# Kernel tuning notes

Measured on AMD Instinct MI355X. Metric: run time of the kernel, lower is better.

## Reference

```python
import jax, jax.numpy as jnp
import numpy as np

MAX_DISP = 48
PATCH = 3
OFFSET = 0
PAD = PATCH // 2
EPS = 1e-3


def _unfold(x, P, pad):
    # x: [B,C,H,W] -> [B,C,K2,H,W], K2 enumerated row-major over the PxP window
    B, C, H, W = x.shape
    xp = jnp.pad(x, ((0, 0), (0, 0), (pad, pad), (pad, pad)))
    return jnp.stack([xp[:, :, i:i + H, j:j + W]
                      for i in range(P) for j in range(P)], axis=2)


def _normalize(x, axes):
    # torch F.normalize: x / clamp(||x||_2, min=eps)
    n = jnp.sqrt(jnp.sum(x * x, axis=axes, keepdims=True))
    return x / jnp.maximum(n, EPS)


def setup_inputs() -> dict:
    key = jax.random.key(0)
    k1, k2, k3 = jax.random.split(key, 3)
    shp = (2, 32, 128, 416)
    return {
        "xl": jax.random.normal(k1, shp, dtype=jnp.float32),
        "xm": jax.random.normal(k2, shp, dtype=jnp.float32),
        "xr": jax.random.normal(k3, shp, dtype=jnp.float32),
    }


def reference(xl, xm, xr):
    B, C, H, W = xl.shape
    K2 = PATCH * PATCH
    scale = (C * K2) ** 0.5

    pl = _normalize(_unfold(xl, PATCH, PAD), (1, 2))  # [B,C,K2,H,W]
    pr = _normalize(_unfold(xr, PATCH, PAD), (1, 2))
    fl = _normalize(xm, (1,))                          # [B,C,H,W]

    # fl is constant over the K2 axis, so sum patches over K2 once for sim_L/sim_R
    Sl = pl.sum(axis=2)  # [B,C,H,W]
    Sr = pr.sum(axis=2)

    cL, cR, cLR = [], [], []
    for d in range(OFFSET, OFFSET + MAX_DISP):
        if d > 0:
            # shifted_l[w] = patches_l[w+d] (zero right pad); shifted_r[w] = patches_r[w-d]
            sL = jnp.einsum('bchw,bchw->bhw', fl[..., :W - d], Sl[..., d:])
            sL = jnp.pad(sL, ((0, 0), (0, 0), (0, d)))
            sR = jnp.einsum('bchw,bchw->bhw', fl[..., d:], Sr[..., :W - d])
            sR = jnp.pad(sR, ((0, 0), (0, 0), (d, 0)))
            wlr = W - 2 * d  # overlap region of the two opposite shifts
            if wlr > 0:
                sLR = jnp.einsum('bckhw,bckhw->bhw', pl[..., 2 * d:], pr[..., :wlr])
                sLR = jnp.pad(sLR, ((0, 0), (0, 0), (d, d)))
            else:
                sLR = jnp.zeros((B, H, W), xl.dtype)
        else:
            sL = jnp.einsum('bchw,bchw->bhw', fl, Sl)
            sR = jnp.einsum('bchw,bchw->bhw', fl, Sr)
            sLR = jnp.einsum('bckhw,bckhw->bhw', pl, pr)
        cL.append(sL / scale)
        cR.append(sR / scale)
        cLR.append(sLR / scale)

    cost = jnp.stack([jnp.stack(cL, 1), jnp.stack(cR, 1), jnp.stack(cLR, 1)], axis=1)
    return jnp.clip(cost, -10.0, 10.0).astype(jnp.float16)  # [B,3,D,H,W]
```

## Files before the change

### kernel.cpp

```cpp
#include <hip/hip_runtime.h>
#include <math.h>

#define B 2
#define C 32
#define H 128
#define W 416
#define D 48
#define HW (H*W)
#define CHW (C*HW)
#define EPSN 1e-3f
#define ISCALE 0.05892556509887896f
#define LSTRH 40
#define NDSP 4
#define DSPL (D / NDSP)

typedef _Float16 half2v __attribute__((ext_vector_type(2)));
typedef _Float16 half4v __attribute__((ext_vector_type(4)));
typedef _Float16 half8v __attribute__((ext_vector_type(8)));

#if defined(__has_builtin)
#if __has_builtin(__builtin_amdgcn_fdot2)
#define FDOT2(a, b, c) __builtin_amdgcn_fdot2((a), (b), (c), false)
#endif
#endif
#ifndef FDOT2
#define FDOT2(a, b, c) ((c) + (float)(a)[0] * (float)(b)[0] + (float)(a)[1] * (float)(b)[1])
#endif

__device__ __forceinline__ float clip10(float x) {
    return fminf(fmaxf(x, -10.0f), 10.0f);
}

__global__ __launch_bounds__(256) void k_sq(const float* __restrict__ xl,
                                            const float* __restrict__ xr,
                                            const float* __restrict__ xm,
                                            float* __restrict__ sql,
                                            float* __restrict__ sqr,
                                            float* __restrict__ inm) {
    int idx = blockIdx.x * 256 + threadIdx.x;
    if (idx >= B * HW) return;
    int b = idx / HW, hw = idx - b * HW;
    const float* pl = xl + (size_t)b * CHW + hw;
    const float* pr = xr + (size_t)b * CHW + hw;
    const float* pm = xm + (size_t)b * CHW + hw;
    float al = 0.f, ar = 0.f, am = 0.f;
#pragma unroll
    for (int c = 0; c < C; ++c) {
        float vl = pl[c * HW], vr = pr[c * HW], vm = pm[c * HW];
        al += vl * vl; ar += vr * vr; am += vm * vm;
    }
    sql[idx] = al;
    sqr[idx] = ar;
    inm[idx] = 1.0f / fmaxf(sqrtf(am), EPSN);
}

__global__ __launch_bounds__(256) void k_norm(const float* __restrict__ sql,
                                              const float* __restrict__ sqr,
                                              float* __restrict__ inl,
                                              float* __restrict__ inr) {
    int idx = blockIdx.x * 256 + threadIdx.x;
    if (idx >= B * HW) return;
    int b = idx / HW, hw = idx - b * HW;
    int h = hw / W, w = hw - h * W;
    float sl = 0.f, sr = 0.f;
#pragma unroll
    for (int di = -1; di <= 1; ++di) {
        int hh = h + di;
        if (hh < 0 || hh >= H) continue;
#pragma unroll
        for (int dj = -1; dj <= 1; ++dj) {
            int ww = w + dj;
            if (ww < 0 || ww >= W) continue;
            int p = b * HW + hh * W + ww;
            sl += sql[p];
            sr += sqr[p];
        }
    }
    inl[idx] = 1.0f / fmaxf(sqrtf(sl), EPSN);
    inr[idx] = 1.0f / fmaxf(sqrtf(sr), EPSN);
}

__global__ __launch_bounds__(256) void k_box(const float* __restrict__ xl,
                                             const float* __restrict__ xr,
                                             _Float16* __restrict__ boxl,
                                             _Float16* __restrict__ boxr) {
    int idx = blockIdx.x * 256 + threadIdx.x;
    int w4 = (idx % (W / 4)) * 4;
    int h = (idx / (W / 4)) % H;
    int rest = idx / (H * (W / 4));
    size_t base = (size_t)rest * HW;
    float4 al = {0.f, 0.f, 0.f, 0.f}, ar = {0.f, 0.f, 0.f, 0.f};
#pragma unroll
    for (int dh = -1; dh <= 1; ++dh) {
        int hh = h + dh;
        if (hh < 0 || hh >= H) continue;
        const float* rl = xl + base + hh * W;
        const float* rr = xr + base + hh * W;
        float4 m = *(const float4*)(rl + w4);
        float lm = (w4 > 0) ? rl[w4 - 1] : 0.f;
        float rm = (w4 + 4 < W) ? rl[w4 + 4] : 0.f;
        al.x += lm + m.x + m.y;  al.y += m.x + m.y + m.z;
        al.z += m.y + m.z + m.w; al.w += m.z + m.w + rm;
        float4 n = *(const float4*)(rr + w4);
        float ln = (w4 > 0) ? rr[w4 - 1] : 0.f;
        float rn = (w4 + 4 < W) ? rr[w4 + 4] : 0.f;
        ar.x += ln + n.x + n.y;  ar.y += n.x + n.y + n.z;
        ar.z += n.y + n.z + n.w; ar.w += n.z + n.w + rn;
    }
    half4v ol = {(_Float16)al.x, (_Float16)al.y, (_Float16)al.z, (_Float16)al.w};
    half4v orr = {(_Float16)ar.x, (_Float16)ar.y, (_Float16)ar.z, (_Float16)ar.w};
    *(half4v*)(boxl + base + h * W + w4) = ol;
    *(half4v*)(boxr + base + h * W + w4) = orr;
}

__device__ __forceinline__ void stage_row_h(const _Float16* __restrict__ gsrc,
                                            _Float16* __restrict__ lds,
                                            int tid, int nthreads) {
    for (int t = tid; t < (W / 4) * C; t += nthreads) {
        int rw = t & 7;
        int cl = (t >> 3) & 7;
        int g  = t >> 6;
        int wg = g % 13;
        int ch = g / 13;
        int c  = ch * 8 + cl;
        int w4 = (wg * 8 + rw) * 4;
        half4v v = *(const half4v*)(gsrc + (size_t)c * HW + w4);
        lds[(w4 + 0) * LSTRH + c] = v[0];
        lds[(w4 + 1) * LSTRH + c] = v[1];
        lds[(w4 + 2) * LSTRH + c] = v[2];
        lds[(w4 + 3) * LSTRH + c] = v[3];
    }
}

__device__ __forceinline__ void stage_row_cvt(const float* __restrict__ gsrc,
                                              _Float16* __restrict__ lds,
                                              int tid, int nthreads) {
    for (int t = tid; t < (W / 4) * C; t += nthreads) {
        int rw = t & 7;
        int cl = (t >> 3) & 7;
        int g  = t >> 6;
        int wg = g % 13;
        int ch = g / 13;
        int c  = ch * 8 + cl;
        int w4 = (wg * 8 + rw) * 4;
        float4 v = *(const float4*)(gsrc + (size_t)c * HW + w4);
        lds[(w4 + 0) * LSTRH + c] = (_Float16)v.x;
        lds[(w4 + 1) * LSTRH + c] = (_Float16)v.y;
        lds[(w4 + 2) * LSTRH + c] = (_Float16)v.z;
        lds[(w4 + 3) * LSTRH + c] = (_Float16)v.w;
    }
}

__device__ __forceinline__ float dot16(const half2v* __restrict__ a,
                                       const _Float16* __restrict__ col) {
    const half8v* c8 = (const half8v*)col;
    float s = 0.f;
#pragma unroll
    for (int q = 0; q < 4; ++q) {
        half8v v = c8[q];
#pragma unroll
        for (int i = 0; i < 4; ++i) {
            half2v p = {v[2 * i], v[2 * i + 1]};
            s = FDOT2(a[4 * q + i], p, s);
        }
    }
    return s;
}

__device__ __forceinline__ void dot16x2(const half2v* __restrict__ a0,
                                        const half2v* __restrict__ a1,
                                        const _Float16* __restrict__ col,
                                        float& r0, float& r1) {
    const half8v* c8 = (const half8v*)col;
    float s0 = 0.f, s1 = 0.f;
#pragma unroll
    for (int q = 0; q < 4; ++q) {
        half8v v = c8[q];
#pragma unroll
        for (int i = 0; i < 4; ++i) {
            half2v p = {v[2 * i], v[2 * i + 1]};
            s0 = FDOT2(a0[4 * q + i], p, s0);
            s1 = FDOT2(a1[4 * q + i], p, s1);
        }
    }
    r0 = s0; r1 = s1;
}

__global__ __launch_bounds__(256) void k_lr(const float* __restrict__ xm,
                                            const _Float16* __restrict__ boxl,
                                            const _Float16* __restrict__ boxr,
                                            const float* __restrict__ inl,
                                            const float* __restrict__ inr,
                                            const float* __restrict__ inm,
                                            float* __restrict__ out) {
    __shared__ _Float16 sB[W * LSTRH];
    __shared__ float sIn[W];
    int tid = threadIdx.x;
    int h = blockIdx.x;
    int b = blockIdx.y;
    int d0 = blockIdx.z * DSPL;
    bool act = tid < (W / 2);
    int w = 2 * tid;
    int bhw = b * HW + h * W;
    const float* pm = xm + (size_t)b * CHW + h * W;

    half2v fl0[C / 2], fl1[C / 2];
    if (act) {
        float2 im = *(const float2*)(inm + bhw + w);
#pragma unroll
        for (int c2 = 0; c2 < C / 2; ++c2) {
            float2 ma = *(const float2*)(pm + (2 * c2) * HW + w);
            float2 mb = *(const float2*)(pm + (2 * c2 + 1) * HW + w);
            half2v f0 = {(_Float16)(ma.x * im.x), (_Float16)(mb.x * im.x)};
            half2v f1 = {(_Float16)(ma.y * im.y), (_Float16)(mb.y * im.y)};
            fl0[c2] = f0; fl1[c2] = f1;
        }
    } else {
#pragma unroll
        for (int c2 = 0; c2 < C / 2; ++c2) {
            half2v z = {(_Float16)0.f, (_Float16)0.f};
            fl0[c2] = z; fl1[c2] = z;
        }
    }

    stage_row_h(boxl + (size_t)b * CHW + h * W, sB, tid, 256);
    for (int j = tid; j < W; j += 256) sIn[j] = inl[bhw + j];
    __syncthreads();
    if (act) {
        float* o = out + ((size_t)b * 3 + 0) * D * HW + h * W;
        float a0p = 0.f;
#pragma unroll 4
        for (int j = 0; j <= DSPL; ++j) {
            int v = w + d0 + j;
            float a0 = 0.f, a1 = 0.f;
            if (v < W) {
                dot16x2(fl0, fl1, sB + v * LSTRH, a0, a1);
                float s = sIn[v] * ISCALE;
                a0 = clip10(a0 * s);
                a1 = clip10(a1 * s);
            }
            if (j >= 1) {
                int d = d0 + j - 1;
                *(float2*)(o + (size_t)d * HW + w) = make_float2(a0p, a1);
            }
            a0p = a0;
        }
    }
    __syncthreads();

    stage_row_h(boxr + (size_t)b * CHW + h * W, sB, tid, 256);
    for (int j = tid; j < W; j += 256) sIn[j] = inr[bhw + j];
    __syncthreads();
    if (act) {
        float* o = out + ((size_t)b * 3 + 1) * D * HW + h * W;
        float a0p = 0.f;
#pragma unroll 4
        for (int j = 0; j <= DSPL; ++j) {
            int v = w - d0 - (DSPL - 1) + j;
            float a0 = 0.f, a1 = 0.f;
            if (v >= 0) {
                dot16x2(fl0, fl1, sB + v * LSTRH, a0, a1);
                float s = sIn[v] * ISCALE;
                a0 = clip10(a0 * s);
                a1 = clip10(a1 * s);
            }
            if (j >= 1) {
                int d = d0 + DSPL - j;
                *(float2*)(o + (size_t)d * HW + w) = make_float2(a0p, a1);
            }
            a0p = a0;
        }
    }
}

__global__ __launch_bounds__(448) void k_e(const float* __restrict__ xl,
                                           const float* __restrict__ xr,
                                           float* __restrict__ EH) {
    __shared__ _Float16 sXL[W * LSTRH];
    int tid = threadIdx.x;
    int h = blockIdx.x;
    int b = blockIdx.y;
    int d0 = blockIdx.z * DSPL;
    int lane = tid & 63;
    int wv = tid >> 6;
    int v = wv * 62 + lane - 1;
    bool vin = (v >= 0) && (v < W);
    const float* br = xr + (size_t)b * CHW + h * W;

    half2v xrv[C / 2];
#pragma unroll
    for (int c2 = 0; c2 < C / 2; ++c2) {
        float va = vin ? br[(2 * c2) * HW + v] : 0.f;
        float vb = vin ? br[(2 * c2 + 1) * HW + v] : 0.f;
        half2v x = {(_Float16)va, (_Float16)vb};
        xrv[c2] = x;
    }

    stage_row_cvt(xl + (size_t)b * CHW + h * W, sXL, tid, 448);
    __syncthreads();

    bool wr = (lane >= 1) && (lane <= 62) && (v < W);
    float* pe = EH + (((size_t)b * D) * H + h) * W + v;
    for (int d = d0; d < d0 + DSPL; ++d) {
        int s = 2 * d;
        float e = 0.0f;
        if (vin && v + s < W) e = dot16(xrv, sXL + (v + s) * LSTRH);
        float em = __shfl_up(e, 1);
        float ep = __shfl_down(e, 1);
        float eh = em + e + ep;
        if (wr) pe[(size_t)d * HW] = eh;
    }
}

#define DCH 12
__global__ __launch_bounds__(448) void k_lr2(const float* __restrict__ EH,
                                             const float* __restrict__ inl,
                                             const float* __restrict__ inr,
                                             float* __restrict__ out) {
    int w = threadIdx.x;
    int dc = blockIdx.x;
    int h = blockIdx.y;
    int b = blockIdx.z;
    if (w >= W) return;
    int bhw = b * HW + h * W;
    bool hm = (h > 0), hp = (h < H - 1);

    float* o = out + ((size_t)b * 3 + 2) * D * HW + h * W + w;
#pragma unroll
    for (int i = 0; i < DCH; ++i) {
        int d = dc * DCH + i;
        float r = 0.0f;
        if (w >= d && w + d < W) {
            int vc = w - d;
            const float* base = EH + ((size_t)b * D + d) * HW + vc;
            float e = base[h * W];
            if (hm) e += base[(h - 1) * W];
            if (hp) e += base[(h + 1) * W];
            float nl = inl[bhw + w + d];
            float nr = inr[bhw + vc];
            r = clip10(e * nl * nr * ISCALE);
        }
        o[(size_t)d * HW] = r;
    }
}

extern "C" void kernel_launch(void* const* d_in, const int* in_sizes, int n_in,
                              void* d_out, int out_size, void* d_ws, size_t ws_size,
                              hipStream_t stream) {
    const float* xl = (const float*)d_in[0];
    const float* xm = (const float*)d_in[1];
    const float* xr = (const float*)d_in[2];
    float* out = (float*)d_out;

    float* ws = (float*)d_ws;
    float* EH   = ws;
    float* inl  = EH + (size_t)B * D * HW;
    float* inr  = inl + B * HW;
    float* inm  = inr + B * HW;
    float* sql  = inm + B * HW;
    float* sqr  = sql + B * HW;
    _Float16* boxl = (_Float16*)(sqr + B * HW);
    _Float16* boxr = boxl + (size_t)B * CHW;

    k_sq<<<dim3((B * HW + 255) / 256), dim3(256), 0, stream>>>(xl, xr, xm, sql, sqr, inm);
    k_norm<<<dim3((B * HW + 255) / 256), dim3(256), 0, stream>>>(sql, sqr, inl, inr);
    k_box<<<dim3((B * CHW / 4 + 255) / 256), dim3(256), 0, stream>>>(xl, xr, boxl, boxr);
    k_e<<<dim3(H, B, NDSP), dim3(448), 0, stream>>>(xl, xr, EH);
    k_lr<<<dim3(H, B, NDSP), dim3(256), 0, stream>>>(xm, boxl, boxr, inl, inr, inm, out);
    k_lr2<<<dim3(4, H, B), dim3(448), 0, stream>>>(EH, inl, inr, out);
}
```

Before: 196.6 us.

## Fuse E and L/R cost kernels, store EH in fp16, restructure LR2 over h

```diff
diff --git a/kernel.cpp b/kernel.cpp
--- a/kernel.cpp
+++ b/kernel.cpp
@@ -13,6 +13,8 @@
 #define LSTRH 40
 #define NDSP 4
 #define DSPL (D / NDSP)
+#define HC 4
+#define HB (H / HC)
 
 typedef _Float16 half2v __attribute__((ext_vector_type(2)));
 typedef _Float16 half4v __attribute__((ext_vector_type(4)));
@@ -167,180 +169,140 @@
     return s;
 }
 
-__device__ __forceinline__ void dot16x2(const half2v* __restrict__ a0,
-                                        const half2v* __restrict__ a1,
-                                        const _Float16* __restrict__ col,
-                                        float& r0, float& r1) {
-    const half8v* c8 = (const half8v*)col;
-    float s0 = 0.f, s1 = 0.f;
-#pragma unroll
-    for (int q = 0; q < 4; ++q) {
-        half8v v = c8[q];
-#pragma unroll
-        for (int i = 0; i < 4; ++i) {
-            half2v p = {v[2 * i], v[2 * i + 1]};
-            s0 = FDOT2(a0[4 * q + i], p, s0);
-            s1 = FDOT2(a1[4 * q + i], p, s1);
-        }
-    }
-    r0 = s0; r1 = s1;
-}
-
-__global__ __launch_bounds__(256) void k_lr(const float* __restrict__ xm,
-                                            const _Float16* __restrict__ boxl,
-                                            const _Float16* __restrict__ boxr,
-                                            const float* __restrict__ inl,
-                                            const float* __restrict__ inr,
-                                            const float* __restrict__ inm,
-                                            float* __restrict__ out) {
+__global__ __launch_bounds__(448) void k_elr(const float* __restrict__ xl,
+                                             const float* __restrict__ xr,
+                                             const float* __restrict__ xm,
+                                             const _Float16* __restrict__ boxl,
+                                             const _Float16* __restrict__ boxr,
+                                             const float* __restrict__ inl,
+                                             const float* __restrict__ inr,
+                                             const float* __restrict__ inm,
+                                             _Float16* __restrict__ EH,
+                                             float* __restrict__ out) {
     __shared__ _Float16 sB[W * LSTRH];
     __shared__ float sIn[W];
     int tid = threadIdx.x;
     int h = blockIdx.x;
     int b = blockIdx.y;
     int d0 = blockIdx.z * DSPL;
-    bool act = tid < (W / 2);
-    int w = 2 * tid;
     int bhw = b * HW + h * W;
-    const float* pm = xm + (size_t)b * CHW + h * W;
-
-    half2v fl0[C / 2], fl1[C / 2];
-    if (act) {
-        float2 im = *(const float2*)(inm + bhw + w);
+
+    {
+        int lane = tid & 63;
+        int wv = tid >> 6;
+        int v = wv * 62 + lane - 1;
+        bool vin = (v >= 0) && (v < W);
+        const float* br = xr + (size_t)b * CHW + h * W;
+
+        half2v xrv[C / 2];
 #pragma unroll
         for (int c2 = 0; c2 < C / 2; ++c2) {
-            float2 ma = *(const float2*)(pm + (2 * c2) * HW + w);
-            float2 mb = *(const float2*)(pm + (2 * c2 + 1) * HW + w);
-            half2v f0 = {(_Float16)(ma.x * im.x), (_Float16)(mb.x * im.x)};
-            half2v f1 = {(_Float16)(ma.y * im.y), (_Float16)(mb.y * im.y)};
-            fl0[c2] = f0; fl1[c2] = f1;
-        }
-    } else {
+            float va = vin ? br[(2 * c2) * HW + v] : 0.f;
+            float vb = vin ? br[(2 * c2 + 1) * HW + v] : 0.f;
+            half2v x = {(_Float16)va, (_Float16)vb};
+            xrv[c2] = x;
+        }
+
+        stage_row_cvt(xl + (size_t)b * CHW + h * W, sB, tid, 448);
+        __syncthreads();
+
+        bool wr = (lane >= 1) && (lane <= 62) && (v < W);
+        _Float16* pe = EH + (((size_t)b * D) * H + h) * W + v;
+        for (int d = d0; d < d0 + DSPL; ++d) {
+            int s = 2 * d;
+            float e = 0.0f;
+            if (vin && v + s < W) e = dot16(xrv, sB + (v + s) * LSTRH);
+            float em = __shfl_up(e, 1);
+            float ep = __shfl_down(e, 1);
+            float eh = em + e + ep;
+            if (wr) pe[(size_t)d * HW] = (_Float16)eh;
+        }
+        __syncthreads();
+    }
+
+    int w = tid;
+    bool act = w < W;
+    half2v fl[C / 2];
+    {
+        const float* pm = xm + (size_t)b * CHW + h * W;
+        float im = act ? inm[bhw + w] : 0.f;
 #pragma unroll
         for (int c2 = 0; c2 < C / 2; ++c2) {
-            half2v z = {(_Float16)0.f, (_Float16)0.f};
-            fl0[c2] = z; fl1[c2] = z;
-        }
-    }
-
-    stage_row_h(boxl + (size_t)b * CHW + h * W, sB, tid, 256);
-    for (int j = tid; j < W; j += 256) sIn[j] = inl[bhw + j];
+            float va = act ? pm[(2 * c2) * HW + w] : 0.f;
+            float vb = act ? pm[(2 * c2 + 1) * HW + w] : 0.f;
+            half2v f = {(_Float16)(va * im), (_Float16)(vb * im)};
+            fl[c2] = f;
+        }
+    }
+
+    stage_row_h(boxl + (size_t)b * CHW + h * W, sB, tid, 448);
+    for (int j = tid; j < W; j += 448) sIn[j] = inl[bhw + j];
     __syncthreads();
     if (act) {
-        float* o = out + ((size_t)b * 3 + 0) * D * HW + h * W;
-        float a0p = 0.f;
-#pragma unroll 4
-        for (int j = 0; j <= DSPL; ++j) {
-            int v = w + d0 + j;
-            float a0 = 0.f, a1 = 0.f;
+        float* o = out + ((size_t)b * 3 + 0) * D * HW + h * W + w;
+        for (int d = d0; d < d0 + DSPL; ++d) {
+            float oL = 0.f;
+            int v = w + d;
             if (v < W) {
-                dot16x2(fl0, fl1, sB + v * LSTRH, a0, a1);
-                float s = sIn[v] * ISCALE;
-                a0 = clip10(a0 * s);
-                a1 = clip10(a1 * s);
+                float a = dot16(fl, sB + v * LSTRH);
+                oL = clip10(a * sIn[v] * ISCALE);
             }
-            if (j >= 1) {
-                int d = d0 + j - 1;
-                *(float2*)(o + (size_t)d * HW + w) = make_float2(a0p, a1);
-            }
-            a0p = a0;
+            o[(size_t)d * HW] = oL;
         }
     }
     __syncthreads();
 
-    stage_row_h(boxr + (size_t)b * CHW + h * W, sB, tid, 256);
-    for (int j = tid; j < W; j += 256) sIn[j] = inr[bhw + j];
+    stage_row_h(boxr + (size_t)b * CHW + h * W, sB, tid, 448);
+    for (int j = tid; j < W; j += 448) sIn[j] = inr[bhw + j];
     __syncthreads();
     if (act) {
-        float* o = out + ((size_t)b * 3 + 1) * D * HW + h * W;
-        float a0p = 0.f;
-#pragma unroll 4
-        for (int j = 0; j <= DSPL; ++j) {
-            int v = w - d0 - (DSPL - 1) + j;
-            float a0 = 0.f, a1 = 0.f;
+        float* o = out + ((size_t)b * 3 + 1) * D * HW + h * W + w;
+        for (int d = d0; d < d0 + DSPL; ++d) {
+            float oR = 0.f;
+            int v = w - d;
             if (v >= 0) {
-                dot16x2(fl0, fl1, sB + v * LSTRH, a0, a1);
-                float s = sIn[v] * ISCALE;
-                a0 = clip10(a0 * s);
-                a1 = clip10(a1 * s);
+                float a = dot16(fl, sB + v * LSTRH);
+                oR = clip10(a * sIn[v] * ISCALE);
             }
-            if (j >= 1) {
-                int d = d0 + DSPL - j;
-                *(float2*)(o + (size_t)d * HW + w) = make_float2(a0p, a1);
-            }
-            a0p = a0;
-        }
-    }
-}
-
-__global__ __launch_bounds__(448) void k_e(const float* __restrict__ xl,
-                                           const float* __restrict__ xr,
-                                           float* __restrict__ EH) {
-    __shared__ _Float16 sXL[W * LSTRH];
-    int tid = threadIdx.x;
-    int h = blockIdx.x;
-    int b = blockIdx.y;
-    int d0 = blockIdx.z * DSPL;
-    int lane = tid & 63;
-    int wv = tid >> 6;
-    int v = wv * 62 + lane - 1;
-    bool vin = (v >= 0) && (v < W);
-    const float* br = xr + (size_t)b * CHW + h * W;
-
-    half2v xrv[C / 2];
-#pragma unroll
-    for (int c2 = 0; c2 < C / 2; ++c2) {
-        float va = vin ? br[(2 * c2) * HW + v] : 0.f;
-        float vb = vin ? br[(2 * c2 + 1) * HW + v] : 0.f;
-        half2v x = {(_Float16)va, (_Float16)vb};
-        xrv[c2] = x;
-    }
-
-    stage_row_cvt(xl + (size_t)b * CHW + h * W, sXL, tid, 448);
-    __syncthreads();
-
-    bool wr = (lane >= 1) && (lane <= 62) && (v < W);
-    float* pe = EH + (((size_t)b * D) * H + h) * W + v;
-    for (int d = d0; d < d0 + DSPL; ++d) {
-        int s = 2 * d;
-        float e = 0.0f;
-        if (vin && v + s < W) e = dot16(xrv, sXL + (v + s) * LSTRH);
-        float em = __shfl_up(e, 1);
-        float ep = __shfl_down(e, 1);
-        float eh = em + e + ep;
-        if (wr) pe[(size_t)d * HW] = eh;
-    }
-}
-
-#define DCH 12
-__global__ __launch_bounds__(448) void k_lr2(const float* __restrict__ EH,
+            o[(size_t)d * HW] = oR;
+        }
+    }
+}
+
+__global__ __launch_bounds__(256) void k_lr2(const _Float16* __restrict__ EH,
                                              const float* __restrict__ inl,
                                              const float* __restrict__ inr,
                                              float* __restrict__ out) {
-    int w = threadIdx.x;
-    int dc = blockIdx.x;
-    int h = blockIdx.y;
-    int b = blockIdx.z;
+    int tid = threadIdx.x;
+    int w = blockIdx.x * 256 + tid;
+    int d = blockIdx.y;
+    int z = blockIdx.z;
+    int b = z / HC, hc = z - b * HC;
     if (w >= W) return;
-    int bhw = b * HW + h * W;
-    bool hm = (h > 0), hp = (h < H - 1);
-
-    float* o = out + ((size_t)b * 3 + 2) * D * HW + h * W + w;
-#pragma unroll
-    for (int i = 0; i < DCH; ++i) {
-        int d = dc * DCH + i;
-        float r = 0.0f;
-        if (w >= d && w + d < W) {
-            int vc = w - d;
-            const float* base = EH + ((size_t)b * D + d) * HW + vc;
-            float e = base[h * W];
-            if (hm) e += base[(h - 1) * W];
-            if (hp) e += base[(h + 1) * W];
-            float nl = inl[bhw + w + d];
-            float nr = inr[bhw + vc];
-            r = clip10(e * nl * nr * ISCALE);
-        }
-        o[(size_t)d * HW] = r;
+    int vc = w - d;
+    bool valid = (vc >= 0) && (w + d < W);
+    int h0 = hc * HB;
+
+    const _Float16* pe = EH + ((size_t)b * D + d) * HW + vc;
+    const float* pl = inl + b * HW + w + d;
+    const float* pr = inr + b * HW + vc;
+    float* o = out + ((size_t)b * 3 + 2) * D * HW + (size_t)d * HW + w;
+
+    float em = 0.f, e0 = 0.f;
+    if (valid) {
+        em = (h0 > 0) ? (float)pe[(h0 - 1) * W] : 0.f;
+        e0 = (float)pe[h0 * W];
+    }
+#pragma unroll 4
+    for (int h = h0; h < h0 + HB; ++h) {
+        float r = 0.f;
+        if (valid) {
+            float ep = (h + 1 < H) ? (float)pe[(h + 1) * W] : 0.f;
+            float e = em + e0 + ep;
+            r = clip10(e * pl[h * W] * pr[h * W] * ISCALE);
+            em = e0; e0 = ep;
+        }
+        o[h * W] = r;
     }
 }
 
@@ -353,19 +315,19 @@
     float* out = (float*)d_out;
 
     float* ws = (float*)d_ws;
-    float* EH   = ws;
-    float* inl  = EH + (size_t)B * D * HW;
+    float* inl  = ws;
     float* inr  = inl + B * HW;
     float* inm  = inr + B * HW;
     float* sql  = inm + B * HW;
     float* sqr  = sql + B * HW;
     _Float16* boxl = (_Float16*)(sqr + B * HW);
     _Float16* boxr = boxl + (size_t)B * CHW;
+    _Float16* EH   = boxr + (size_t)B * CHW;
 
     k_sq<<<dim3((B * HW + 255) / 256), dim3(256), 0, stream>>>(xl, xr, xm, sql, sqr, inm);
     k_norm<<<dim3((B * HW + 255) / 256), dim3(256), 0, stream>>>(sql, sqr, inl, inr);
     k_box<<<dim3((B * CHW / 4 + 255) / 256), dim3(256), 0, stream>>>(xl, xr, boxl, boxr);
-    k_e<<<dim3(H, B, NDSP), dim3(448), 0, stream>>>(xl, xr, EH);
-    k_lr<<<dim3(H, B, NDSP), dim3(256), 0, stream>>>(xm, boxl, boxr, inl, inr, inm, out);
-    k_lr2<<<dim3(4, H, B), dim3(448), 0, stream>>>(EH, inl, inr, out);
-}
+    k_elr<<<dim3(H, B, NDSP), dim3(448), 0, stream>>>(xl, xr, xm, boxl, boxr,
+                                                      inl, inr, inm, EH, out);
+    k_lr2<<<dim3(2, D, B * HC), dim3(256), 0, stream>>>(EH, inl, inr, out);
+}
```

Result: slower. 205.6 us (+4.6%).
